# Optimization experiments

Hardware: AMD Instinct MI355X
Metric: run time of the kernel (lower is better)

Reference implementation:

```python
import jax, jax.numpy as jnp
import numpy as np

N_STATE, N_OBS, BATCH, T_LEN = 256, 128, 64, 1024
RICCATI_ITERS = 300


def _steady_state_gain(A, H, Q, R, iters=RICCATI_ITERS):
    """Riccati iteration for the steady-state Kalman gain (numpy, fp64)."""
    n = A.shape[0]
    I = np.eye(n)
    P = np.eye(n)
    for _ in range(iters):
        Pp = A @ P @ A.T + Q
        S = H @ Pp @ H.T + R
        K = np.linalg.solve(S, (Pp @ H.T).T).T
        P = (I - K @ H) @ Pp
    return K


def setup_inputs() -> dict:
    rng = np.random.default_rng(0)
    # Stable dynamics: scaled orthogonal matrix (spectral radius 0.95).
    M = rng.standard_normal((N_STATE, N_STATE))
    Qm, _ = np.linalg.qr(M)
    A = 0.95 * Qm
    H = rng.standard_normal((N_OBS, N_STATE)) / np.sqrt(N_STATE)
    Qc = 0.1 * np.eye(N_STATE)
    Rc = 0.1 * np.eye(N_OBS)
    K = _steady_state_gain(A, H, Qc, Rc)

    key = jax.random.key(0)
    y = jax.random.normal(key, (BATCH, T_LEN, N_OBS), dtype=jnp.float32)
    return {
        "y": y,
        "A": jnp.asarray(A, dtype=jnp.float32),
        "H": jnp.asarray(H, dtype=jnp.float32),
        "K": jnp.asarray(K, dtype=jnp.float32),
    }


def reference(y, A, H, K):
    """Steady-state Kalman filter: x_t = (I - K H) A x_{t-1} + K y_t.

    y: [B, T, n_obs] -> out: [B, T, n_state]
    """
    n = A.shape[0]
    I = jnp.eye(n, dtype=A.dtype)
    A_eff = (I - K @ H) @ A  # [n, n]

    x0 = y[:, 0] @ K.T  # [B, n]

    def step(x, yt):
        x = x @ A_eff.T + yt @ K.T  # [B, n]
        return x, x

    ys = jnp.swapaxes(y[:, 1:], 0, 1)  # [T-1, B, n_obs]
    _, xs = jax.lax.scan(step, x0, ys)  # xs: [T-1, B, n]
    out = jnp.concatenate([x0[:, None, :], jnp.swapaxes(xs, 0, 1)], axis=1)
    return out  # [B, T, n_state]
```

## Files before the change

kernel.cpp:

```cpp
#include <hip/hip_runtime.h>
#include <hip/hip_bf16.h>

#define NS 256
#define MO 128
#define BB 64
#define TT 1024

typedef short s16x8 __attribute__((ext_vector_type(8)));
typedef float f32x4 __attribute__((ext_vector_type(4)));
typedef unsigned int uint;
typedef unsigned short ushort;

__device__ __forceinline__ ushort f2bf(float x) {
    uint u = __float_as_uint(x);
    uint r = (u + 0x7fffu + ((u >> 16) & 1u)) >> 16;
    return (ushort)r;
}
__device__ __forceinline__ float bf2f(ushort h) { return __uint_as_float(((uint)h) << 16); }

__device__ __forceinline__ uint pkbf2(float a, float b) {
    __hip_bfloat162 h = __float22bfloat162_rn(make_float2(a, b));
    union { __hip_bfloat162 b2; uint u; } cv;
    cv.b2 = h;
    return cv.u;
}

__device__ __forceinline__ void conv8(float4 f0, float4 f1, s16x8& vh, s16x8& vl) {
    uint h0 = pkbf2(f0.x, f0.y), h1 = pkbf2(f0.z, f0.w);
    uint h2 = pkbf2(f1.x, f1.y), h3 = pkbf2(f1.z, f1.w);
    float r0 = f0.x - __uint_as_float(h0 << 16);
    float r1 = f0.y - __uint_as_float(h0 & 0xffff0000u);
    float r2 = f0.z - __uint_as_float(h1 << 16);
    float r3 = f0.w - __uint_as_float(h1 & 0xffff0000u);
    float r4 = f1.x - __uint_as_float(h2 << 16);
    float r5 = f1.y - __uint_as_float(h2 & 0xffff0000u);
    float r6 = f1.z - __uint_as_float(h3 << 16);
    float r7 = f1.w - __uint_as_float(h3 & 0xffff0000u);
    uint l0 = pkbf2(r0, r1), l1 = pkbf2(r2, r3);
    uint l2 = pkbf2(r4, r5), l3 = pkbf2(r6, r7);
    union { uint u[4]; s16x8 v; } ch, cl;
    ch.u[0] = h0; ch.u[1] = h1; ch.u[2] = h2; ch.u[3] = h3;
    cl.u[0] = l0; cl.u[1] = l1; cl.u[2] = l2; cl.u[3] = l3;
    vh = ch.v; vl = cl.v;
}

__device__ __forceinline__ f32x4 mfma16(s16x8 a, s16x8 b, f32x4 c) {
    return __builtin_amdgcn_mfma_f32_16x16x32_bf16(a, b, c, 0, 0, 0);
}


__global__ void khaeff_kernel(const float* __restrict__ K, const float* __restrict__ H,
                              const float* __restrict__ A, float* __restrict__ AE,
                              ushort* __restrict__ kbh, ushort* __restrict__ kbl,
                              ushort* __restrict__ aeh, ushort* __restrict__ ael) {
    int i = blockIdx.x, j = threadIdx.x;
    __shared__ float kl[MO];
    __shared__ float khr[NS];
    if (j < MO) {
        float v = K[i * MO + j];
        kl[j] = v;
        ushort hi = f2bf(v);
        kbh[i * MO + j] = hi;
        kbl[i * MO + j] = f2bf(v - bf2f(hi));
    }
    __syncthreads();
    float acc = 0.f;
#pragma unroll 8
    for (int k = 0; k < MO; ++k) acc += kl[k] * H[k * NS + j];
    khr[j] = acc;
    __syncthreads();
    float ae = A[i * NS + j];
#pragma unroll 8
    for (int k = 0; k < NS; ++k) ae -= khr[k] * A[k * NS + j];
    AE[i * NS + j] = ae;
    ushort hi = f2bf(ae);
    aeh[i * NS + j] = hi;
    ael[i * NS + j] = f2bf(ae - bf2f(hi));
}

__global__ void matsq_kernel(const float* __restrict__ src, float* __restrict__ dst,
                             ushort* dh, ushort* dl) {
    int i = blockIdx.x, j = threadIdx.x;
    __shared__ float row[NS];
    row[j] = src[i * NS + j];
    __syncthreads();
    float acc = 0.f;
#pragma unroll 8
    for (int k = 0; k < NS; ++k) acc += row[k] * src[k * NS + j];
    dst[i * NS + j] = acc;
    if (dh) {
        ushort hi = f2bf(acc);
        dh[i * NS + j] = hi;
        dl[i * NS + j] = f2bf(acc - bf2f(hi));
    }
}


template <int MODE>
__launch_bounds__(512, 2)
__global__ void scan16_kernel(const ushort* __restrict__ mh, const ushort* __restrict__ ml,
                              const ushort* __restrict__ kah, const ushort* __restrict__ kal,
                              const float* __restrict__ y_g, const ushort* __restrict__ ub,
                              const ushort* __restrict__ cin, float* outf,
                              ushort* __restrict__ wbf, ushort* __restrict__ ebf) {
    constexpr int S = (MODE == 2) ? 15 : ((MODE == 3) ? 7 : 8);
    constexpr bool YF = (MODE == 0 || MODE == 4);
    const int tid = threadIdx.x, blk = blockIdx.x;
    const int w = tid >> 6, l = tid & 63, lr = l & 15, lg = l >> 4;

    __shared__ ushort xh_s[2][16 * NS];
    __shared__ ushort xl_s[2][16 * NS];

    s16x8 Bh[2][8], Bl[2][8];
#pragma unroll
    for (int t2 = 0; t2 < 2; ++t2) {
        int row = 16 * (2 * w + t2) + lr;
#pragma unroll
        for (int q = 0; q < 8; ++q) {
            int off = row * NS + 32 * q + 8 * lg;
            Bh[t2][q] = *(const s16x8*)(mh + off);
            Bl[t2][q] = *(const s16x8*)(ml + off);
        }
    }

    s16x8 KAh[2][4], KAl[2][4];
    if constexpr (YF) {
#pragma unroll
        for (int t2 = 0; t2 < 2; ++t2) {
            int row = 16 * (2 * w + t2) + lr;
#pragma unroll
            for (int q = 0; q < 4; ++q) {
                int off = row * MO + 32 * q + 8 * lg;
                KAh[t2][q] = *(const s16x8*)(kah + off);
                KAl[t2][q] = *(const s16x8*)(kal + off);
            }
        }
    }

    const int b0 = (blk & 3) * 16;
    const int cc = blk >> 2;

#pragma unroll
    for (int jj = 0; jj < 8; ++jj) {
        int idx = jj * 512 + tid;
        int m = idx >> 8, col = idx & 255;
        ushort hu = 0;
        if constexpr (MODE == 3) {
            hu = cin[((long)blk * 16 + m) * NS + col];
            wbf[((long)blk * 128 + 8 * m) * NS + col] = hu;
        } else if constexpr (MODE == 4) {
            hu = cin[((long)(b0 + m) * 128 + cc) * NS + col];
        } else if constexpr (MODE == 2) {
            wbf[((long)(blk * 16 + m) * 16) * NS + col] = 0;
        }
        int si = (m * NS + col) ^ ((m & 7) << 3);
        xh_s[0][si] = hu;
        xl_s[0][si] = 0;
    }

    const int st0 = 32 * w + 4 * lg;
    const int st1 = st0 + 16;

    long ybase = 0, ubase = 0;
    if constexpr (YF) {
        ybase = ((long)(b0 + lr) * TT + cc * 8) * MO + 8 * lg;
    } else if constexpr (MODE == 1 || MODE == 3) {
        ubase = ((long)blk * 128 + 8 * lr) * NS;
    } else {
        ubase = ((long)(blk * 16 + lr) * 16) * NS;
    }

    auto ldu = [&](long off) -> f32x4 {
        uint2 v = *(const uint2*)(ub + off);
        return f32x4{__uint_as_float(v.x << 16), __uint_as_float(v.x & 0xffff0000u),
                     __uint_as_float(v.y << 16), __uint_as_float(v.y & 0xffff0000u)};
    };

    auto compute_u = [&](int s, f32x4& ua0, f32x4& ua1) {
        ua0 = f32x4{0.f, 0.f, 0.f, 0.f};
        ua1 = f32x4{0.f, 0.f, 0.f, 0.f};
#pragma unroll
        for (int q = 0; q < 4; ++q) {
            long off = ybase + (long)s * MO + 32 * q;
            float4 f0 = *(const float4*)(y_g + off);
            float4 f1 = *(const float4*)(y_g + off + 4);
            s16x8 yh, yl;
            conv8(f0, f1, yh, yl);
            ua0 = mfma16(KAh[0][q], yh, ua0);
            ua0 = mfma16(KAl[0][q], yh, ua0);
            ua0 = mfma16(KAh[0][q], yl, ua0);
            ua1 = mfma16(KAh[1][q], yh, ua1);
            ua1 = mfma16(KAl[1][q], yh, ua1);
            ua1 = mfma16(KAh[1][q], yl, ua1);
        }
    };

    f32x4 up0, up1;
    if constexpr (YF) {
        compute_u(0, up0, up1);
    } else {
        up0 = ldu(ubase + st0);
        up1 = ldu(ubase + st1);
    }
    __syncthreads();

    for (int s = 0; s < S; ++s) {
        const int cur = s & 1, nxt = cur ^ 1;
        f32x4 acc0 = up0, acc1 = up1;

#pragma unroll
        for (int q = 0; q < 8; ++q) {
            int ridx = (lr * NS + 32 * q + 8 * lg) ^ ((lr & 7) << 3);
            s16x8 xh = *(const s16x8*)&xh_s[cur][ridx];
            s16x8 xl = *(const s16x8*)&xl_s[cur][ridx];
            acc0 = mfma16(Bh[0][q], xh, acc0);
            acc0 = mfma16(Bh[0][q], xl, acc0);
            acc0 = mfma16(Bl[0][q], xh, acc0);
            acc1 = mfma16(Bh[1][q], xh, acc1);
            acc1 = mfma16(Bh[1][q], xl, acc1);
            acc1 = mfma16(Bl[1][q], xh, acc1);
        }

        if (s + 1 < S) {
            if constexpr (YF) {
                compute_u(s + 1, up0, up1);
            } else {
                up0 = ldu(ubase + (long)(s + 1) * NS + st0);
                up1 = ldu(ubase + (long)(s + 1) * NS + st1);
            }
        }

        uint h01a = pkbf2(acc0[0], acc0[1]), h23a = pkbf2(acc0[2], acc0[3]);
        uint h01b = pkbf2(acc1[0], acc1[1]), h23b = pkbf2(acc1[2], acc1[3]);

        if constexpr (MODE == 2) {
            long wb = ((long)(blk * 16 + lr) * 16 + s + 1) * NS;
            *(uint2*)(wbf + wb + st0) = make_uint2(h01a, h23a);
            *(uint2*)(wbf + wb + st1) = make_uint2(h01b, h23b);
        } else if constexpr (MODE == 3) {
            long wb = ((long)blk * 128 + 8 * lr + s + 1) * NS;
            *(uint2*)(wbf + wb + st0) = make_uint2(h01a, h23a);
            *(uint2*)(wbf + wb + st1) = make_uint2(h01b, h23b);
        } else if constexpr (MODE == 4) {
            long ob = ((long)(b0 + lr) * TT + cc * 8 + s) * NS;
            *(f32x4*)(outf + ob + st0) = acc0;
            *(f32x4*)(outf + ob + st1) = acc1;
        } else if constexpr (MODE == 0) {
            if (s == S - 1) {
                long eb = ((long)(b0 + lr) * 128 + cc) * NS;
                *(uint2*)(ebf + eb + st0) = make_uint2(h01a, h23a);
                *(uint2*)(ebf + eb + st1) = make_uint2(h01b, h23b);
            }
        } else if constexpr (MODE == 1) {
            if (s == S - 1) {
                long eb = ((long)blk * 16 + lr) * NS;
                *(uint2*)(ebf + eb + st0) = make_uint2(h01a, h23a);
                *(uint2*)(ebf + eb + st1) = make_uint2(h01b, h23b);
            }
        }

        if (s + 1 < S) {
            float la0 = acc0[0] - __uint_as_float(h01a << 16);
            float la1 = acc0[1] - __uint_as_float(h01a & 0xffff0000u);
            float la2 = acc0[2] - __uint_as_float(h23a << 16);
            float la3 = acc0[3] - __uint_as_float(h23a & 0xffff0000u);
            float lb0 = acc1[0] - __uint_as_float(h01b << 16);
            float lb1 = acc1[1] - __uint_as_float(h01b & 0xffff0000u);
            float lb2 = acc1[2] - __uint_as_float(h23b << 16);
            float lb3 = acc1[3] - __uint_as_float(h23b & 0xffff0000u);
            int wi0 = lr * NS + (st0 ^ ((lr & 7) << 3));
            int wi1 = lr * NS + (st1 ^ ((lr & 7) << 3));
            *(uint2*)&xh_s[nxt][wi0] = make_uint2(h01a, h23a);
            *(uint2*)&xh_s[nxt][wi1] = make_uint2(h01b, h23b);
            *(uint2*)&xl_s[nxt][wi0] = make_uint2(pkbf2(la0, la1), pkbf2(la2, la3));
            *(uint2*)&xl_s[nxt][wi1] = make_uint2(pkbf2(lb0, lb1), pkbf2(lb2, lb3));
        }
        __syncthreads();
    }
}


extern "C" void kernel_launch(void* const* d_in, const int* in_sizes, int n_in,
                              void* d_out, int out_size, void* d_ws, size_t ws_size,
                              hipStream_t stream) {
    const float* y = (const float*)d_in[0];
    const float* A = (const float*)d_in[1];
    const float* H = (const float*)d_in[2];
    const float* K = (const float*)d_in[3];
    float* out = (float*)d_out;

    float* ws = (float*)d_ws;
    const long MAT = (long)NS * NS;
    float* AE = ws + 0 * MAT;
    float* Ta = ws + 1 * MAT;
    float* Tb = ws + 2 * MAT;
    float* M8 = ws + 3 * MAT;
    float* M64 = ws + 4 * MAT;
    ushort* aeh = (ushort*)(ws + 5 * MAT);
    ushort* ael = aeh + MAT;
    ushort* mh = (ushort*)(ws + 6 * MAT);
    ushort* ml = mh + MAT;
    ushort* m2h = (ushort*)(ws + 7 * MAT);
    ushort* m2l = m2h + MAT;
    ushort* kbh = (ushort*)(ws + 8 * MAT);
    ushort* kbl = kbh + (long)NS * MO;
    ushort* e_buf = (ushort*)(ws + 9 * MAT);
    ushort* cbuf = (ushort*)(ws + 25 * MAT);
    ushort* e2 = (ushort*)(ws + 41 * MAT);
    ushort* c2 = (ushort*)(ws + 43 * MAT);

    khaeff_kernel<<<NS, NS, 0, stream>>>(K, H, A, AE, kbh, kbl, aeh, ael);
    matsq_kernel<<<NS, NS, 0, stream>>>(AE, Ta, nullptr, nullptr);
    matsq_kernel<<<NS, NS, 0, stream>>>(Ta, Tb, nullptr, nullptr);
    matsq_kernel<<<NS, NS, 0, stream>>>(Tb, M8, mh, ml);
    matsq_kernel<<<NS, NS, 0, stream>>>(M8, Ta, nullptr, nullptr);
    matsq_kernel<<<NS, NS, 0, stream>>>(Ta, Tb, nullptr, nullptr);
    matsq_kernel<<<NS, NS, 0, stream>>>(Tb, M64, m2h, m2l);

    scan16_kernel<0><<<512, 512, 0, stream>>>(aeh, ael, kbh, kbl, y, nullptr, nullptr, nullptr, nullptr, e_buf);
    scan16_kernel<1><<<64, 512, 0, stream>>>(mh, ml, nullptr, nullptr, nullptr, e_buf, nullptr, nullptr, nullptr, e2);
    scan16_kernel<2><<<4, 512, 0, stream>>>(m2h, m2l, nullptr, nullptr, nullptr, e2, nullptr, nullptr, c2, nullptr);
    scan16_kernel<3><<<64, 512, 0, stream>>>(mh, ml, nullptr, nullptr, nullptr, e_buf, c2, nullptr, cbuf, nullptr);
    scan16_kernel<4><<<512, 512, 0, stream>>>(aeh, ael, kbh, kbl, y, nullptr, cbuf, out, nullptr, nullptr);
}
```

Baseline: 282.8 us.

## Restructure hierarchical scan to 16-step chunks, drop K low-part, prefetch y

Changes the chunked parallel scan hierarchy from 8-step chunks over 128 chunks to 16-step chunks over 64 chunks. Power matrices move from A^8/A^64 to A^16/A^128, and the level-1/2/3 index maps are rewritten to match. The K split-bf16 low part is dropped, so u=K*y uses two MFMAs instead of three. y loads for the next step are now issued before the recurrence MFMAs to hide latency. Fewer blocks and longer sequential chunks reduce parallelism, and dropping K's low part lowers precision.

```diff
diff --git a/kernel.cpp b/kernel.cpp
--- a/kernel.cpp
+++ b/kernel.cpp
@@ -51,7 +51,7 @@
 
 __global__ void khaeff_kernel(const float* __restrict__ K, const float* __restrict__ H,
                               const float* __restrict__ A, float* __restrict__ AE,
-                              ushort* __restrict__ kbh, ushort* __restrict__ kbl,
+                              ushort* __restrict__ kah,
                               ushort* __restrict__ aeh, ushort* __restrict__ ael) {
     int i = blockIdx.x, j = threadIdx.x;
     __shared__ float kl[MO];
@@ -59,9 +59,7 @@
     if (j < MO) {
         float v = K[i * MO + j];
         kl[j] = v;
-        ushort hi = f2bf(v);
-        kbh[i * MO + j] = hi;
-        kbl[i * MO + j] = f2bf(v - bf2f(hi));
+        kah[i * MO + j] = f2bf(v);
     }
     __syncthreads();
     float acc = 0.f;
@@ -99,12 +97,12 @@
 template <int MODE>
 __launch_bounds__(512, 2)
 __global__ void scan16_kernel(const ushort* __restrict__ mh, const ushort* __restrict__ ml,
-                              const ushort* __restrict__ kah, const ushort* __restrict__ kal,
+                              const ushort* __restrict__ kah,
                               const float* __restrict__ y_g, const ushort* __restrict__ ub,
                               const ushort* __restrict__ cin, float* outf,
                               ushort* __restrict__ wbf, ushort* __restrict__ ebf) {
-    constexpr int S = (MODE == 2) ? 15 : ((MODE == 3) ? 7 : 8);
     constexpr bool YF = (MODE == 0 || MODE == 4);
+    constexpr int S = YF ? 16 : ((MODE == 1) ? 8 : 7);
     const int tid = threadIdx.x, blk = blockIdx.x;
     const int w = tid >> 6, l = tid & 63, lr = l & 15, lg = l >> 4;
 
@@ -123,16 +121,14 @@
         }
     }
 
-    s16x8 KAh[2][4], KAl[2][4];
+    s16x8 KAh[2][4];
     if constexpr (YF) {
 #pragma unroll
         for (int t2 = 0; t2 < 2; ++t2) {
             int row = 16 * (2 * w + t2) + lr;
 #pragma unroll
             for (int q = 0; q < 4; ++q) {
-                int off = row * MO + 32 * q + 8 * lg;
-                KAh[t2][q] = *(const s16x8*)(kah + off);
-                KAl[t2][q] = *(const s16x8*)(kal + off);
+                KAh[t2][q] = *(const s16x8*)(kah + row * MO + 32 * q + 8 * lg);
             }
         }
     }
@@ -146,12 +142,14 @@
         int m = idx >> 8, col = idx & 255;
         ushort hu = 0;
         if constexpr (MODE == 3) {
-            hu = cin[((long)blk * 16 + m) * NS + col];
-            wbf[((long)blk * 128 + 8 * m) * NS + col] = hu;
+            int rid = blk * 16 + m;
+            int b = rid >> 3, g = rid & 7;
+            hu = cin[((long)b * 8 + g) * NS + col];
+            wbf[((long)b * 64 + 8 * g) * NS + col] = hu;
         } else if constexpr (MODE == 4) {
-            hu = cin[((long)(b0 + m) * 128 + cc) * NS + col];
+            hu = cin[((long)(b0 + m) * 64 + cc) * NS + col];
         } else if constexpr (MODE == 2) {
-            wbf[((long)(blk * 16 + m) * 16) * NS + col] = 0;
+            wbf[(long)(blk * 16 + m) * 8 * NS + col] = 0;
         }
         int si = (m * NS + col) ^ ((m & 7) << 3);
         xh_s[0][si] = hu;
@@ -163,11 +161,12 @@
 
     long ybase = 0, ubase = 0;
     if constexpr (YF) {
-        ybase = ((long)(b0 + lr) * TT + cc * 8) * MO + 8 * lg;
+        ybase = ((long)(b0 + lr) * TT + cc * 16) * MO + 8 * lg;
     } else if constexpr (MODE == 1 || MODE == 3) {
-        ubase = ((long)blk * 128 + 8 * lr) * NS;
+        int rid = blk * 16 + lr;
+        ubase = ((long)(rid >> 3) * 64 + 8 * (rid & 7)) * NS;
     } else {
-        ubase = ((long)(blk * 16 + lr) * 16) * NS;
+        ubase = (long)(blk * 16 + lr) * 8 * NS;
     }
 
     auto ldu = [&](long off) -> f32x4 {
@@ -176,28 +175,34 @@
                      __uint_as_float(v.y << 16), __uint_as_float(v.y & 0xffff0000u)};
     };
 
-    auto compute_u = [&](int s, f32x4& ua0, f32x4& ua1) {
+    float4 yraw[8];
+    auto load_y = [&](int s) {
+#pragma unroll
+        for (int q = 0; q < 4; ++q) {
+            long off = ybase + (long)s * MO + 32 * q;
+            yraw[2 * q] = *(const float4*)(y_g + off);
+            yraw[2 * q + 1] = *(const float4*)(y_g + off + 4);
+        }
+    };
+
+    auto compute_u = [&](f32x4& ua0, f32x4& ua1) {
         ua0 = f32x4{0.f, 0.f, 0.f, 0.f};
         ua1 = f32x4{0.f, 0.f, 0.f, 0.f};
 #pragma unroll
         for (int q = 0; q < 4; ++q) {
-            long off = ybase + (long)s * MO + 32 * q;
-            float4 f0 = *(const float4*)(y_g + off);
-            float4 f1 = *(const float4*)(y_g + off + 4);
             s16x8 yh, yl;
-            conv8(f0, f1, yh, yl);
+            conv8(yraw[2 * q], yraw[2 * q + 1], yh, yl);
             ua0 = mfma16(KAh[0][q], yh, ua0);
-            ua0 = mfma16(KAl[0][q], yh, ua0);
             ua0 = mfma16(KAh[0][q], yl, ua0);
             ua1 = mfma16(KAh[1][q], yh, ua1);
-            ua1 = mfma16(KAl[1][q], yh, ua1);
             ua1 = mfma16(KAh[1][q], yl, ua1);
         }
     };
 
     f32x4 up0, up1;
     if constexpr (YF) {
-        compute_u(0, up0, up1);
+        load_y(0);
+        compute_u(up0, up1);
     } else {
         up0 = ldu(ubase + st0);
         up1 = ldu(ubase + st1);
@@ -206,6 +211,11 @@
 
     for (int s = 0; s < S; ++s) {
         const int cur = s & 1, nxt = cur ^ 1;
+
+        if constexpr (YF) {
+            if (s + 1 < S) load_y(s + 1);
+        }
+
         f32x4 acc0 = up0, acc1 = up1;
 
 #pragma unroll
@@ -223,7 +233,7 @@
 
         if (s + 1 < S) {
             if constexpr (YF) {
-                compute_u(s + 1, up0, up1);
+                compute_u(up0, up1);
             } else {
                 up0 = ldu(ubase + (long)(s + 1) * NS + st0);
                 up1 = ldu(ubase + (long)(s + 1) * NS + st1);
@@ -234,26 +244,28 @@
         uint h01b = pkbf2(acc1[0], acc1[1]), h23b = pkbf2(acc1[2], acc1[3]);
 
         if constexpr (MODE == 2) {
-            long wb = ((long)(blk * 16 + lr) * 16 + s + 1) * NS;
+            long wb = ((long)(blk * 16 + lr) * 8 + s + 1) * NS;
             *(uint2*)(wbf + wb + st0) = make_uint2(h01a, h23a);
             *(uint2*)(wbf + wb + st1) = make_uint2(h01b, h23b);
         } else if constexpr (MODE == 3) {
-            long wb = ((long)blk * 128 + 8 * lr + s + 1) * NS;
+            int rid = blk * 16 + lr;
+            long wb = ((long)(rid >> 3) * 64 + 8 * (rid & 7) + s + 1) * NS;
             *(uint2*)(wbf + wb + st0) = make_uint2(h01a, h23a);
             *(uint2*)(wbf + wb + st1) = make_uint2(h01b, h23b);
         } else if constexpr (MODE == 4) {
-            long ob = ((long)(b0 + lr) * TT + cc * 8 + s) * NS;
+            long ob = ((long)(b0 + lr) * TT + cc * 16 + s) * NS;
             *(f32x4*)(outf + ob + st0) = acc0;
             *(f32x4*)(outf + ob + st1) = acc1;
         } else if constexpr (MODE == 0) {
             if (s == S - 1) {
-                long eb = ((long)(b0 + lr) * 128 + cc) * NS;
+                long eb = ((long)(b0 + lr) * 64 + cc) * NS;
                 *(uint2*)(ebf + eb + st0) = make_uint2(h01a, h23a);
                 *(uint2*)(ebf + eb + st1) = make_uint2(h01b, h23b);
             }
         } else if constexpr (MODE == 1) {
             if (s == S - 1) {
-                long eb = ((long)blk * 16 + lr) * NS;
+                int rid = blk * 16 + lr;
+                long eb = ((long)(rid >> 3) * 8 + (rid & 7)) * NS;
                 *(uint2*)(ebf + eb + st0) = make_uint2(h01a, h23a);
                 *(uint2*)(ebf + eb + st1) = make_uint2(h01b, h23b);
             }
@@ -294,32 +306,31 @@
     float* AE = ws + 0 * MAT;
     float* Ta = ws + 1 * MAT;
     float* Tb = ws + 2 * MAT;
-    float* M8 = ws + 3 * MAT;
-    float* M64 = ws + 4 * MAT;
-    ushort* aeh = (ushort*)(ws + 5 * MAT);
+    ushort* us = (ushort*)(ws + 3 * MAT);
+    ushort* aeh = us;
     ushort* ael = aeh + MAT;
-    ushort* mh = (ushort*)(ws + 6 * MAT);
+    ushort* mh = ael + MAT;
     ushort* ml = mh + MAT;
-    ushort* m2h = (ushort*)(ws + 7 * MAT);
+    ushort* m2h = ml + MAT;
     ushort* m2l = m2h + MAT;
-    ushort* kbh = (ushort*)(ws + 8 * MAT);
-    ushort* kbl = kbh + (long)NS * MO;
-    ushort* e_buf = (ushort*)(ws + 9 * MAT);
-    ushort* cbuf = (ushort*)(ws + 25 * MAT);
-    ushort* e2 = (ushort*)(ws + 41 * MAT);
-    ushort* c2 = (ushort*)(ws + 43 * MAT);
-
-    khaeff_kernel<<<NS, NS, 0, stream>>>(K, H, A, AE, kbh, kbl, aeh, ael);
+    ushort* kah = m2l + MAT;
+    ushort* e_buf = kah + (long)NS * MO;
+    ushort* cbuf = e_buf + (long)BB * 64 * NS;
+    ushort* e2 = cbuf + (long)BB * 64 * NS;
+    ushort* c2 = e2 + (long)BB * 8 * NS;
+
+    khaeff_kernel<<<NS, NS, 0, stream>>>(K, H, A, AE, kah, aeh, ael);
     matsq_kernel<<<NS, NS, 0, stream>>>(AE, Ta, nullptr, nullptr);
     matsq_kernel<<<NS, NS, 0, stream>>>(Ta, Tb, nullptr, nullptr);
-    matsq_kernel<<<NS, NS, 0, stream>>>(Tb, M8, mh, ml);
-    matsq_kernel<<<NS, NS, 0, stream>>>(M8, Ta, nullptr, nullptr);
+    matsq_kernel<<<NS, NS, 0, stream>>>(Tb, Ta, nullptr, nullptr);
+    matsq_kernel<<<NS, NS, 0, stream>>>(Ta, Tb, mh, ml);
+    matsq_kernel<<<NS, NS, 0, stream>>>(Tb, Ta, nullptr, nullptr);
     matsq_kernel<<<NS, NS, 0, stream>>>(Ta, Tb, nullptr, nullptr);
-    matsq_kernel<<<NS, NS, 0, stream>>>(Tb, M64, m2h, m2l);
-
-    scan16_kernel<0><<<512, 512, 0, stream>>>(aeh, ael, kbh, kbl, y, nullptr, nullptr, nullptr, nullptr, e_buf);
-    scan16_kernel<1><<<64, 512, 0, stream>>>(mh, ml, nullptr, nullptr, nullptr, e_buf, nullptr, nullptr, nullptr, e2);
-    scan16_kernel<2><<<4, 512, 0, stream>>>(m2h, m2l, nullptr, nullptr, nullptr, e2, nullptr, nullptr, c2, nullptr);
-    scan16_kernel<3><<<64, 512, 0, stream>>>(mh, ml, nullptr, nullptr, nullptr, e_buf, c2, nullptr, cbuf, nullptr);
-    scan16_kernel<4><<<512, 512, 0, stream>>>(aeh, ael, kbh, kbl, y, nullptr, cbuf, out, nullptr, nullptr);
-}
+    matsq_kernel<<<NS, NS, 0, stream>>>(Tb, Ta, m2h, m2l);
+
+    scan16_kernel<0><<<256, 512, 0, stream>>>(aeh, ael, kah, y, nullptr, nullptr, nullptr, nullptr, e_buf);
+    scan16_kernel<1><<<32, 512, 0, stream>>>(mh, ml, nullptr, nullptr, e_buf, nullptr, nullptr, nullptr, e2);
+    scan16_kernel<2><<<4, 512, 0, stream>>>(m2h, m2l, nullptr, nullptr, e2, nullptr, nullptr, c2, nullptr);
+    scan16_kernel<3><<<32, 512, 0, stream>>>(mh, ml, nullptr, nullptr, e_buf, c2, nullptr, cbuf, nullptr);
+    scan16_kernel<4><<<256, 512, 0, stream>>>(aeh, ael, kah, y, nullptr, cbuf, out, nullptr, nullptr);
+}
```

Measured after the change: 259.0 us. 8.4% less time.
